# Kernel optimization log

Hardware: AMD Instinct MI355X
Metric: run time of the kernel (lower is better)

The kernel has to match this reference:

```python
import jax, jax.numpy as jnp
import numpy as np

M_B, M_S, D_IN, D_OUT = 4, 2048, 4096, 4096
SPARSITY_KEEP = 0.1


def setup_inputs() -> dict:
    key = jax.random.key(0)
    k1, k2, k3, k4 = jax.random.split(key, 4)
    data = jax.random.normal(k1, (M_B, M_S, D_IN), dtype=jnp.float32)
    weight = jax.random.normal(k2, (D_OUT, D_IN), dtype=jnp.float32) * 0.02
    w_mask = (jax.random.uniform(k3, (D_OUT, D_IN)) < SPARSITY_KEEP).astype(jnp.float32)
    bias_p = jax.random.normal(k4, (D_OUT,), dtype=jnp.float32) * 0.02
    return {"data": data, "weight": weight, "w_mask": w_mask, "bias_p": bias_p}


def reference(data, weight, w_mask, bias_p):
    # Equivalent math to CSR-conversion + sparse GEMM: out = data @ (W*mask)^T + b
    w = weight * w_mask                      # [D_OUT, D_IN]
    out = jnp.einsum('bsk,nk->bsn', data, w)  # [B, S, D_OUT]
    return out + bias_p
```

## Files before the change

kernel.cpp:

```cpp
#include <hip/hip_runtime.h>
#include <hip/hip_bf16.h>


#define M_TOT 8192
#define N_TOT 4096
#define K_TOT 4096

typedef __attribute__((ext_vector_type(8))) short short8;
typedef __attribute__((ext_vector_type(4))) float floatx4;

__device__ inline unsigned short f2bf(float f) {
    unsigned int u = __builtin_bit_cast(unsigned int, f);
    u += 0x7fffu + ((u >> 16) & 1u);
    return (unsigned short)(u >> 16);
}

__global__ __launch_bounds__(256) void cast_data_kernel(const float4* __restrict__ in,
                                                        ushort4* __restrict__ out) {
    int i = blockIdx.x * 256 + threadIdx.x;
    float4 f = in[i];
    ushort4 o;
    o.x = f2bf(f.x); o.y = f2bf(f.y); o.z = f2bf(f.z); o.w = f2bf(f.w);
    out[i] = o;
}

__global__ __launch_bounds__(256) void cast_w_kernel(const float4* __restrict__ w,
                                                     const float4* __restrict__ m,
                                                     ushort4* __restrict__ out) {
    int i = blockIdx.x * 256 + threadIdx.x;
    float4 a = w[i];
    float4 b = m[i];
    ushort4 o;
    o.x = f2bf(a.x * b.x); o.y = f2bf(a.y * b.y);
    o.z = f2bf(a.z * b.z); o.w = f2bf(a.w * b.w);
    out[i] = o;
}

__device__ inline void load_lds16(const unsigned short* g, unsigned short* l) {
    __builtin_amdgcn_global_load_lds(
        (__attribute__((address_space(1))) void*)(const_cast<unsigned short*>(g)),
        (__attribute__((address_space(3))) void*)(l),
        16, 0, 0);
}

__global__ __launch_bounds__(256) void gemm_bt_kernel(const unsigned short* __restrict__ A,
                                                      const unsigned short* __restrict__ W,
                                                      const float* __restrict__ bias,
                                                      float* __restrict__ out) {
    __shared__ __align__(16) unsigned short As[128 * 32];
    __shared__ __align__(16) unsigned short Bs[128 * 32];

    const int t = threadIdx.x;
    const int m0 = blockIdx.y * 128;
    const int n0 = blockIdx.x * 128;

    const int kc = ((t & 3) ^ ((t >> 3) & 3));
    const unsigned short* ag0 = A + (m0 + (t >> 2)) * K_TOT + kc * 8;
    const unsigned short* ag1 = ag0 + 64 * K_TOT;
    const unsigned short* bg0 = W + (n0 + (t >> 2)) * K_TOT + kc * 8;
    const unsigned short* bg1 = bg0 + 64 * K_TOT;
    unsigned short* al0 = As + t * 8;
    unsigned short* al1 = As + t * 8 + 2048;
    unsigned short* bl0 = Bs + t * 8;
    unsigned short* bl1 = Bs + t * 8 + 2048;

    const int wave = t >> 6;
    const int lane = t & 63;
    const int quad = lane >> 4;
    const int row16 = lane & 15;
    const int wm = (wave >> 1) * 64;
    const int wn = (wave & 1) * 64;
    const int xs = (row16 >> 1) & 3;
    const int slot = (quad ^ xs) * 8;

    floatx4 acc[4][4];
#pragma unroll
    for (int i = 0; i < 4; i++)
#pragma unroll
        for (int j = 0; j < 4; j++) {
            floatx4 z = {0.0f, 0.0f, 0.0f, 0.0f};
            acc[i][j] = z;
        }

    for (int kt = 0; kt < K_TOT / 32; ++kt) {
        load_lds16(ag0, al0);
        load_lds16(ag1, al1);
        load_lds16(bg0, bl0);
        load_lds16(bg1, bl1);
        ag0 += 32; ag1 += 32; bg0 += 32; bg1 += 32;
        __syncthreads();

        short8 af[4], bf[4];
#pragma unroll
        for (int i = 0; i < 4; i++) {
            af[i] = *(const short8*)(As + (wm + i * 16 + row16) * 32 + slot);
            bf[i] = *(const short8*)(Bs + (wn + i * 16 + row16) * 32 + slot);
        }
#pragma unroll
        for (int i = 0; i < 4; i++)
#pragma unroll
            for (int j = 0; j < 4; j++)
                acc[i][j] = __builtin_amdgcn_mfma_f32_16x16x32_bf16(af[i], bf[j], acc[i][j], 0, 0, 0);
        __syncthreads();
    }

    float bb[4];
#pragma unroll
    for (int j = 0; j < 4; j++)
        bb[j] = bias[n0 + wn + j * 16 + row16];

#pragma unroll
    for (int i = 0; i < 4; i++) {
        const int gm = m0 + wm + i * 16 + quad * 4;
#pragma unroll
        for (int j = 0; j < 4; j++) {
            const int gn = n0 + wn + j * 16 + row16;
            float* o = out + gm * N_TOT + gn;
#pragma unroll
            for (int r = 0; r < 4; r++)
                o[r * N_TOT] = acc[i][j][r] + bb[j];
        }
    }
}

extern "C" void kernel_launch(void* const* d_in, const int* in_sizes, int n_in,
                              void* d_out, int out_size, void* d_ws, size_t ws_size,
                              hipStream_t stream) {
    const float* data   = (const float*)d_in[0];
    const float* weight = (const float*)d_in[1];
    const float* w_mask = (const float*)d_in[2];
    const float* bias_p = (const float*)d_in[3];
    float* out = (float*)d_out;

    unsigned short* a_bf = (unsigned short*)d_ws;
    unsigned short* w_bf = a_bf + (size_t)M_TOT * K_TOT;

    cast_data_kernel<<<(M_TOT * K_TOT) / (256 * 4), 256, 0, stream>>>(
        (const float4*)data, (ushort4*)a_bf);
    cast_w_kernel<<<(N_TOT * K_TOT) / (256 * 4), 256, 0, stream>>>(
        (const float4*)weight, (const float4*)w_mask, (ushort4*)w_bf);

    dim3 grid(N_TOT / 128, M_TOT / 128);
    gemm_bt_kernel<<<grid, 256, 0, stream>>>(a_bf, w_bf, bias_p, out);
}
```

Before: 610.2 us.

## Rewrite GEMM as 256x256x64 double-buffered pipeline with interleaved LDS loads

Grows the GEMM block tile from 128x128x32 to 256x256x64 with 512 threads (8 waves, each computing a 128x64 sub-tile). Global-to-LDS loads are double-buffered two tiles ahead and split into quarter-sized stages placed between MFMA quarters, using explicit barriers, waitcnt and priority hints. The aim is more data reuse per LDS byte and hiding memory latency behind matrix math. The cost is more registers (128 accumulator floats per lane) and 128KB of LDS per block, which limits occupancy, and a fragile hand-written synchronization schedule.

Result: faster. 564.0 us (-7.6%).

```diff
diff --git a/kernel.cpp b/kernel.cpp
--- a/kernel.cpp
+++ b/kernel.cpp
@@ -5,6 +5,11 @@
 #define M_TOT 8192
 #define N_TOT 4096
 #define K_TOT 4096
+
+#define BM 256
+#define BN 256
+#define BK 64
+#define NT (K_TOT / BK)
 
 typedef __attribute__((ext_vector_type(8))) short short8;
 typedef __attribute__((ext_vector_type(4))) float floatx4;
@@ -43,66 +48,129 @@
         16, 0, 0);
 }
 
-__global__ __launch_bounds__(256) void gemm_bt_kernel(const unsigned short* __restrict__ A,
-                                                      const unsigned short* __restrict__ W,
-                                                      const float* __restrict__ bias,
-                                                      float* __restrict__ out) {
-    __shared__ __align__(16) unsigned short As[128 * 32];
-    __shared__ __align__(16) unsigned short Bs[128 * 32];
+#define BAR()   __builtin_amdgcn_s_barrier()
+#define SB0()   __builtin_amdgcn_sched_barrier(0)
+#define LGKM0() do { asm volatile("s_waitcnt lgkmcnt(0)" ::: "memory"); SB0(); } while (0)
+#define VM8()   asm volatile("s_waitcnt vmcnt(8)" ::: "memory")
+#define VM0()   asm volatile("s_waitcnt vmcnt(0)" ::: "memory")
+
+__global__ __launch_bounds__(512, 2) void gemm_bt_kernel(const unsigned short* __restrict__ A,
+                                                         const unsigned short* __restrict__ W,
+                                                         const float* __restrict__ bias,
+                                                         float* __restrict__ out) {
+    __shared__ __align__(16) unsigned short As[2 * BM * BK];
+    __shared__ __align__(16) unsigned short Bs[2 * BN * BK];
 
     const int t = threadIdx.x;
-    const int m0 = blockIdx.y * 128;
-    const int n0 = blockIdx.x * 128;
-
-    const int kc = ((t & 3) ^ ((t >> 3) & 3));
-    const unsigned short* ag0 = A + (m0 + (t >> 2)) * K_TOT + kc * 8;
-    const unsigned short* ag1 = ag0 + 64 * K_TOT;
-    const unsigned short* bg0 = W + (n0 + (t >> 2)) * K_TOT + kc * 8;
-    const unsigned short* bg1 = bg0 + 64 * K_TOT;
-    unsigned short* al0 = As + t * 8;
-    unsigned short* al1 = As + t * 8 + 2048;
-    unsigned short* bl0 = Bs + t * 8;
-    unsigned short* bl1 = Bs + t * 8 + 2048;
-
-    const int wave = t >> 6;
-    const int lane = t & 63;
-    const int quad = lane >> 4;
+    const int m0 = blockIdx.y * BM;
+    const int n0 = blockIdx.x * BN;
+
+    const int lane  = t & 63;
+    const int wv    = t >> 6;
+    const int wm    = (wv >> 2) * 128;
+    const int wn    = (wv & 3) * 64;
     const int row16 = lane & 15;
-    const int wm = (wave >> 1) * 64;
-    const int wn = (wave & 1) * 64;
-    const int xs = (row16 >> 1) & 3;
-    const int slot = (quad ^ xs) * 8;
-
-    floatx4 acc[4][4];
-#pragma unroll
-    for (int i = 0; i < 4; i++)
+    const int quad  = lane >> 4;
+    const int rx    = row16 & 7;
+
+    const int srow  = t >> 3;
+    const int lslot = (t & 7) ^ (srow & 7);
+    const size_t thr_off = (size_t)srow * K_TOT + (size_t)lslot * 8;
+
+    const unsigned short* Ag = A + (size_t)m0 * K_TOT + thr_off;
+    const unsigned short* Bg = W + (size_t)n0 * K_TOT + thr_off;
+
+    auto stageA = [&](int ts, int h) {
+        const unsigned short* s = Ag + (size_t)(h * 128) * K_TOT + ts * BK;
+        unsigned short* d = As + (ts & 1) * (BM * BK) + h * (128 * BK) + t * 8;
+        load_lds16(s, d);
+        load_lds16(s + (size_t)64 * K_TOT, d + 512 * 8);
+    };
+    auto stageB = [&](int ts, int h) {
+        const unsigned short* s = Bg + (size_t)(h * 128) * K_TOT + ts * BK;
+        unsigned short* d = Bs + (ts & 1) * (BN * BK) + h * (128 * BK) + t * 8;
+        load_lds16(s, d);
+        load_lds16(s + (size_t)64 * K_TOT, d + 512 * 8);
+    };
+
+    short8 af[4][2];
+    short8 bf[2][2][2];
+
+    auto readA_half = [&](int buf, int mh) {
+#pragma unroll
+        for (int i = 0; i < 4; i++) {
+            const unsigned short* base =
+                As + buf * (BM * BK) + (wm + mh * 64 + i * 16 + row16) * BK;
+            af[i][0] = *(const short8*)(base + ((quad ^ rx) << 3));
+            af[i][1] = *(const short8*)(base + (((4 + quad) ^ rx) << 3));
+        }
+    };
+    auto readB_all = [&](int buf) {
+#pragma unroll
+        for (int nh = 0; nh < 2; nh++)
+#pragma unroll
+            for (int j = 0; j < 2; j++) {
+                const unsigned short* base =
+                    Bs + buf * (BN * BK) + (wn + nh * 32 + j * 16 + row16) * BK;
+                bf[nh][j][0] = *(const short8*)(base + ((quad ^ rx) << 3));
+                bf[nh][j][1] = *(const short8*)(base + (((4 + quad) ^ rx) << 3));
+            }
+    };
+
+    floatx4 acc[8][4];
+#pragma unroll
+    for (int i = 0; i < 8; i++)
 #pragma unroll
         for (int j = 0; j < 4; j++) {
             floatx4 z = {0.0f, 0.0f, 0.0f, 0.0f};
             acc[i][j] = z;
         }
 
-    for (int kt = 0; kt < K_TOT / 32; ++kt) {
-        load_lds16(ag0, al0);
-        load_lds16(ag1, al1);
-        load_lds16(bg0, bl0);
-        load_lds16(bg1, bl1);
-        ag0 += 32; ag1 += 32; bg0 += 32; bg1 += 32;
-        __syncthreads();
-
-        short8 af[4], bf[4];
-#pragma unroll
-        for (int i = 0; i < 4; i++) {
-            af[i] = *(const short8*)(As + (wm + i * 16 + row16) * 32 + slot);
-            bf[i] = *(const short8*)(Bs + (wn + i * 16 + row16) * 32 + slot);
-        }
+    auto mmaQ = [&](int mh, int nh) {
+        __builtin_amdgcn_s_setprio(1);
 #pragma unroll
         for (int i = 0; i < 4; i++)
 #pragma unroll
-            for (int j = 0; j < 4; j++)
-                acc[i][j] = __builtin_amdgcn_mfma_f32_16x16x32_bf16(af[i], bf[j], acc[i][j], 0, 0, 0);
-        __syncthreads();
-    }
+            for (int j = 0; j < 2; j++)
+#pragma unroll
+                for (int ks = 0; ks < 2; ks++)
+                    acc[mh * 4 + i][nh * 2 + j] = __builtin_amdgcn_mfma_f32_16x16x32_bf16(
+                        af[i][ks], bf[nh][j][ks], acc[mh * 4 + i][nh * 2 + j], 0, 0, 0);
+        __builtin_amdgcn_s_setprio(0);
+    };
+
+    auto tile = [&](int kt, int mode) {
+        const int buf = kt & 1;
+        readA_half(buf, 0);
+        readB_all(buf);
+        BAR(); LGKM0();
+        mmaQ(0, 0);
+        BAR();
+        if (mode == 0) stageB(kt + 2, 0);
+        BAR(); SB0();
+        mmaQ(0, 1);
+        BAR();
+        readA_half(buf, 1);
+        if (mode == 0) stageB(kt + 2, 1);
+        BAR(); LGKM0();
+        mmaQ(1, 1);
+        BAR();
+        if (mode == 0) { stageA(kt + 2, 0); stageA(kt + 2, 1); VM8(); }
+        if (mode == 1) { VM0(); }
+        BAR(); SB0();
+        mmaQ(1, 0);
+        if (mode != 2) BAR();
+    };
+
+    stageB(0, 0); stageB(0, 1); stageA(0, 0); stageA(0, 1);
+    stageB(1, 0); stageB(1, 1); stageA(1, 0); stageA(1, 1);
+    VM8();
+    BAR();
+
+    for (int kt = 0; kt < NT - 2; ++kt)
+        tile(kt, 0);
+    tile(NT - 2, 1);
+    tile(NT - 1, 2);
 
     float bb[4];
 #pragma unroll
@@ -110,15 +178,15 @@
         bb[j] = bias[n0 + wn + j * 16 + row16];
 
 #pragma unroll
-    for (int i = 0; i < 4; i++) {
-        const int gm = m0 + wm + i * 16 + quad * 4;
-#pragma unroll
-        for (int j = 0; j < 4; j++) {
-            const int gn = n0 + wn + j * 16 + row16;
-            float* o = out + gm * N_TOT + gn;
+    for (int ai = 0; ai < 8; ai++) {
+        const int gm = m0 + wm + ai * 16 + quad * 4;
+#pragma unroll
+        for (int bj = 0; bj < 4; bj++) {
+            const int gn = n0 + wn + bj * 16 + row16;
+            float* o = out + (size_t)gm * N_TOT + gn;
 #pragma unroll
             for (int r = 0; r < 4; r++)
-                o[r * N_TOT] = acc[i][j][r] + bb[j];
+                o[(size_t)r * N_TOT] = acc[ai][bj][r] + bb[bj];
         }
     }
 }
@@ -140,6 +208,6 @@
     cast_w_kernel<<<(N_TOT * K_TOT) / (256 * 4), 256, 0, stream>>>(
         (const float4*)weight, (const float4*)w_mask, (ushort4*)w_bf);
 
-    dim3 grid(N_TOT / 128, M_TOT / 128);
-    gemm_bt_kernel<<<grid, 256, 0, stream>>>(a_bf, w_bf, bias_p, out);
-}
+    dim3 grid(N_TOT / BN, M_TOT / BM);
+    gemm_bt_kernel<<<grid, 512, 0, stream>>>(a_bf, w_bf, bias_p, out);
+}
```
